# Performance work log

Hardware: AMD Instinct MI355X
Metric: run time of the kernel (lower is better)

## Reference

```python
import jax, jax.numpy as jnp
import numpy as np

TAU = 0.5  # config.tau
EPS = 1e-12  # F.normalize eps


def _pair_idx(n_i, hi):
    # all pairs (i, j) with i in [0, n_i), j in (i, hi)
    ii, jj = [], []
    for i in range(n_i):
        js = np.arange(i + 1, hi)
        ii.append(np.full(js.shape, i))
        jj.append(js)
    return np.concatenate(ii), np.concatenate(jj)


def setup_inputs() -> dict:
    key = jax.random.key(0)
    ks = jax.random.split(key, 7)
    B, D, H = 512, 768, 256
    s = 0.02
    return {
        "emb_in": jax.random.normal(ks[0], (B, D), jnp.float32),
        "W1": jax.random.normal(ks[1], (H, 2 * D), jnp.float32) * s,
        "b1": jax.random.normal(ks[2], (H,), jnp.float32) * s,
        "W2": jax.random.normal(ks[3], (H, H), jnp.float32) * s,
        "b2": jax.random.normal(ks[4], (H,), jnp.float32) * s,
        "W3": jax.random.normal(ks[5], (1, H), jnp.float32) * s,
        "b3": jax.random.normal(ks[6], (1,), jnp.float32) * s,
    }


def reference(emb_in, W1, b1, W2, b2, W3, b3):
    B, D = emb_in.shape
    n = B // 4
    m = B // 2

    # L2 normalize rows (torch F.normalize)
    z = emb_in / jnp.maximum(jnp.linalg.norm(emb_in, axis=1, keepdims=True), EPS)
    # cosine similarity matrix [B, B]
    S = z @ z.T

    # ---- ContrastiveLoss (NT-Xent style over first n rows) ----
    logits = S / jnp.asarray(TAU, emb_in.dtype)
    not_diag = 1.0 - jnp.eye(B, dtype=emb_in.dtype)
    denom = jnp.sum(not_diag * jnp.exp(logits), axis=1)  # sum_{k != i} exp(S[i,k]/T)
    log_denom = jnp.log(denom)  # [B]
    ci, cj = _pair_idx(n, n)  # pairs i < j < n
    # loss_ij = -log( exp(S[i,j]/T) / denom_i ) = log_denom[i] - logits[i, j]
    closs_sum = jnp.sum(log_denom[ci] - logits[ci, cj])
    closs = (-2.0 * (n - 1) / n) * closs_sum

    # ---- en_loss: pairwise concat + tiny MLP + BCEWithLogits ----
    ei_np, ej_np = _pair_idx(n, B)  # pairs i in [0,n), j in (i, B)
    ei = jnp.asarray(ei_np)
    ej = jnp.asarray(ej_np)
    labels = (ej_np < m).astype(np.float32)  # first m-(i+1) pairs per i are positives
    labels = jnp.asarray(labels)

    x = jnp.concatenate([z[ei], z[ej]], axis=1)  # [P, 2D]
    h1 = jax.nn.relu(x @ W1.T + b1)              # [P, H]
    h2 = jax.nn.relu(h1 @ W2.T + b2)             # [P, H]
    logit = (h2 @ W3.T + b3)[:, 0]               # [P]

    # BCEWithLogitsLoss (mean), numerically stable form
    bce = jnp.maximum(logit, 0.0) - logit * labels + jnp.log1p(jnp.exp(-jnp.abs(logit)))
    eloss = jnp.mean(bce)

    return closs + eloss
```

## Files before the change

kernel.cpp:

```cpp
#include <hip/hip_runtime.h>
#include <hip/hip_bf16.h>
#include <math.h>

#define B 512
#define D 768
#define H 256
#define NN 128
#define MM 256
#define P_PAIRS 57280
#define NPBLK 895

typedef __attribute__((ext_vector_type(8))) __bf16 bf16x8;
typedef __attribute__((ext_vector_type(4))) __bf16 bf16x4;
typedef __attribute__((ext_vector_type(4))) float f32x4;


__global__ __launch_bounds__(256) void k_prep(const float* __restrict__ emb,
                                              const float* __restrict__ W1,
                                              const float* __restrict__ W2,
                                              __bf16* __restrict__ zbf,
                                              __bf16* __restrict__ W1b,
                                              __bf16* __restrict__ W2b) {
    int bx = blockIdx.x;
    int t = threadIdx.x;
    if (bx < B) {
        float4 v4 = make_float4(0.f, 0.f, 0.f, 0.f);
        float ss = 0.f;
        if (t < D / 4) {
            v4 = *(const float4*)(emb + bx * D + 4 * t);
            ss = v4.x * v4.x + v4.y * v4.y + v4.z * v4.z + v4.w * v4.w;
        }
        __shared__ float red[256];
        red[t] = ss;
        __syncthreads();
        for (int s = 128; s > 0; s >>= 1) {
            if (t < s) red[t] += red[t + s];
            __syncthreads();
        }
        float inv = 1.0f / fmaxf(sqrtf(red[0]), 1e-12f);
        if (t < D / 4) {
            bf16x4 o;
            o[0] = (__bf16)(v4.x * inv); o[1] = (__bf16)(v4.y * inv);
            o[2] = (__bf16)(v4.z * inv); o[3] = (__bf16)(v4.w * inv);
            *(bf16x4*)(zbf + bx * D + 4 * t) = o;
        }
    } else if (bx < B + 64) {
        int e4 = (bx - B) * 256 + t;
        float4 w = *(const float4*)(W2 + 4 * e4);
        bf16x4 o;
        o[0] = (__bf16)w.x; o[1] = (__bf16)w.y; o[2] = (__bf16)w.z; o[3] = (__bf16)w.w;
        *(bf16x4*)(W2b + 4 * e4) = o;
    } else {
        int n = bx - B - 64;
        if (t < D / 4) {
            float4 w = *(const float4*)(W1 + (n & 255) * (2 * D) + (n >> 8) * D + 4 * t);
            bf16x4 o;
            o[0] = (__bf16)w.x; o[1] = (__bf16)w.y; o[2] = (__bf16)w.z; o[3] = (__bf16)w.w;
            *(bf16x4*)(W1b + n * D + 4 * t) = o;
        }
    }
}

__global__ __launch_bounds__(128) void k_sim_uv(const __bf16* __restrict__ zbf,
                                                const __bf16* __restrict__ W1b,
                                                const float* __restrict__ b1,
                                                __bf16* __restrict__ Up,
                                                __bf16* __restrict__ Vv,
                                                float* __restrict__ esp,
                                                float* __restrict__ slp) {
    int bx = blockIdx.x;
    int w = threadIdx.x >> 6;
    int lane = threadIdx.x & 63;
    int r = lane & 15, q = lane >> 4;

    if (bx < 32) {
        int m0 = (bx >> 2) * 16;
        int n0 = (bx & 3) * 128 + w * 64;
        int slot = (bx & 3) * 2 + w;
        f32x4 acc[4] = {};
        const __bf16* Ab = zbf + (m0 + r) * D + 8 * q;
        #pragma unroll 4
        for (int s = 0; s < D / 32; s++) {
            bf16x8 a = *(const bf16x8*)(Ab + 32 * s);
            #pragma unroll
            for (int nt = 0; nt < 4; nt++) {
                bf16x8 b = *(const bf16x8*)(zbf + (n0 + 16 * nt + r) * D + 8 * q + 32 * s);
                acc[nt] = __builtin_amdgcn_mfma_f32_16x16x32_bf16(a, b, acc[nt], 0, 0, 0);
            }
        }
        #pragma unroll
        for (int rr = 0; rr < 4; rr++) {
            int irow = m0 + q * 4 + rr;
            float es = 0.f, sl = 0.f;
            #pragma unroll
            for (int nt = 0; nt < 4; nt++) {
                int kcol = n0 + nt * 16 + r;
                float C = acc[nt][rr];
                if (kcol != irow) es += expf(2.f * C);
                if (kcol > irow && kcol < NN) sl += 2.f * C;
            }
            #pragma unroll
            for (int m = 1; m <= 8; m <<= 1) {
                es += __shfl_xor(es, m);
                sl += __shfl_xor(sl, m);
            }
            if (r == 0) {
                esp[slot * NN + irow] = es;
                slp[slot * NN + irow] = sl;
            }
        }
    } else {
        int bxu = bx - 32;
        int m0 = (bxu >> 3) * 32 + 16 * w;
        int n0 = (bxu & 7) * 64;
        f32x4 acc[4] = {};
        const __bf16* Ab = zbf + (m0 + r) * D + 8 * q;
        #pragma unroll 4
        for (int s = 0; s < D / 32; s++) {
            bf16x8 a = *(const bf16x8*)(Ab + 32 * s);
            #pragma unroll
            for (int nt = 0; nt < 4; nt++) {
                bf16x8 b = *(const bf16x8*)(W1b + (n0 + 16 * nt + r) * D + 8 * q + 32 * s);
                acc[nt] = __builtin_amdgcn_mfma_f32_16x16x32_bf16(a, b, acc[nt], 0, 0, 0);
            }
        }
        #pragma unroll
        for (int nt = 0; nt < 4; nt++) {
            int n = n0 + 16 * nt + r;
            float bias = (n < H) ? b1[n] : 0.f;
            #pragma unroll
            for (int rr = 0; rr < 4; rr++) {
                int m = m0 + 4 * q + rr;
                float C = acc[nt][rr] + bias;
                if (n < H) Up[m * H + n] = (__bf16)C;
                else       Vv[m * H + (n - H)] = (__bf16)C;
            }
        }
    }
}

__global__ __launch_bounds__(256, 2) void k_pairs(const __bf16* __restrict__ Up,
                                                  const __bf16* __restrict__ Vv,
                                                  const __bf16* __restrict__ W2b,
                                                  const float* __restrict__ b2,
                                                  const float* __restrict__ W3,
                                                  const float* __restrict__ b3,
                                                  float* __restrict__ bcepart) {
    __shared__ __bf16 h1[64][264];
    __shared__ int jj_s[64];
    __shared__ float redbuf[4][64];

    int tid = threadIdx.x;
    int w = tid >> 6, lane = tid & 63;
    int r = lane & 15, q = lane >> 4;
    int p0 = blockIdx.x * 64;

    if (tid < 64) {
        int p = p0 + tid;
        float disc = 1046529.f - 8.f * (float)p;
        int i = (int)((1023.f - sqrtf(disc)) * 0.5f);
        if (i < 0) i = 0;
        if (i > NN - 1) i = NN - 1;
        while (i > 0 && i * (1023 - i) / 2 > p) i--;
        while ((i + 1) * (1022 - i) / 2 <= p) i++;
        int j = i + 1 + (p - i * (1023 - i) / 2);
        jj_s[tid] = (i << 16) | j;
    }
    __syncthreads();

    {
        int t = tid & 63, g = tid >> 6;
        int ij = jj_s[t];
        int i = ij >> 16, j = ij & 0xffff;
        const __bf16* up = Up + i * H + 64 * g;
        const __bf16* vp = Vv + j * H + 64 * g;
        #pragma unroll
        for (int c8 = 0; c8 < 8; c8++) {
            bf16x8 u8 = *(const bf16x8*)(up + 8 * c8);
            bf16x8 v8 = *(const bf16x8*)(vp + 8 * c8);
            bf16x8 hv;
            #pragma unroll
            for (int e = 0; e < 8; e++)
                hv[e] = (__bf16)fmaxf((float)u8[e] + (float)v8[e], 0.f);
            *(bf16x8*)&h1[t][64 * g + 8 * c8] = hv;
        }
    }
    __syncthreads();

    f32x4 acc[4][4] = {};
    const __bf16* wb = W2b + (64 * w + r) * H + 8 * q;
    #pragma unroll
    for (int s = 0; s < 8; s++) {
        bf16x8 a[4], b[4];
        #pragma unroll
        for (int mt = 0; mt < 4; mt++)
            a[mt] = *(const bf16x8*)&h1[16 * mt + r][32 * s + 8 * q];
        #pragma unroll
        for (int nt = 0; nt < 4; nt++)
            b[nt] = *(const bf16x8*)(wb + 16 * nt * H + 32 * s);
        #pragma unroll
        for (int mt = 0; mt < 4; mt++)
            #pragma unroll
            for (int nt = 0; nt < 4; nt++)
                acc[mt][nt] = __builtin_amdgcn_mfma_f32_16x16x32_bf16(a[mt], b[nt], acc[mt][nt], 0, 0, 0);
    }

    float part[4][4] = {};
    #pragma unroll
    for (int nt = 0; nt < 4; nt++) {
        int n = 64 * w + 16 * nt + r;
        float b2v = b2[n], w3v = W3[n];
        #pragma unroll
        for (int mt = 0; mt < 4; mt++)
            #pragma unroll
            for (int rr = 0; rr < 4; rr++) {
                float h2 = fmaxf(acc[mt][nt][rr] + b2v, 0.f);
                part[mt][rr] += h2 * w3v;
            }
    }
    #pragma unroll
    for (int mt = 0; mt < 4; mt++)
        #pragma unroll
        for (int rr = 0; rr < 4; rr++) {
            float v = part[mt][rr];
            #pragma unroll
            for (int m = 1; m <= 8; m <<= 1) v += __shfl_xor(v, m);
            if (r == 0) redbuf[w][16 * mt + 4 * q + rr] = v;
        }
    __syncthreads();

    if (tid < 64) {
        int j = jj_s[tid] & 0xffff;
        float logit = redbuf[0][tid] + redbuf[1][tid] +
                      redbuf[2][tid] + redbuf[3][tid] + b3[0];
        float label = (j < MM) ? 1.f : 0.f;
        float lsum = fmaxf(logit, 0.f) - logit * label +
                     log1pf(expf(-fabsf(logit)));
        #pragma unroll
        for (int off = 32; off > 0; off >>= 1) lsum += __shfl_down(lsum, off);
        if (tid == 0) bcepart[blockIdx.x] = lsum;
    }
}

__global__ __launch_bounds__(256) void k_final(const float* __restrict__ esp,
                                               const float* __restrict__ slp,
                                               const float* __restrict__ bcepart,
                                               float* __restrict__ out) {
    __shared__ float red[256];
    int t = threadIdx.x;

    float s = 0.f;
    for (int p = t; p < NPBLK; p += 256) s += bcepart[p];
    red[t] = s;
    __syncthreads();
    for (int st = 128; st > 0; st >>= 1) {
        if (t < st) red[t] += red[t + st];
        __syncthreads();
    }
    float bce_total = red[0];
    __syncthreads();

    float v = 0.f;
    if (t < NN) {
        float es = 0.f, sl = 0.f;
        #pragma unroll
        for (int s8 = 0; s8 < 8; s8++) {
            es += esp[s8 * NN + t];
            sl += slp[s8 * NN + t];
        }
        v = (float)(NN - 1 - t) * logf(es) - sl;
    }
    red[t] = v;
    __syncthreads();
    for (int st = 128; st > 0; st >>= 1) {
        if (t < st) red[t] += red[t + st];
        __syncthreads();
    }
    if (t == 0) {
        float closs = (-2.0f * (float)(NN - 1) / (float)NN) * red[0];
        out[0] = closs + bce_total / (float)P_PAIRS;
    }
}

extern "C" void kernel_launch(void* const* d_in, const int* in_sizes, int n_in,
                              void* d_out, int out_size, void* d_ws, size_t ws_size,
                              hipStream_t stream) {
    const float* emb = (const float*)d_in[0];
    const float* W1  = (const float*)d_in[1];
    const float* b1  = (const float*)d_in[2];
    const float* W2  = (const float*)d_in[3];
    const float* b2  = (const float*)d_in[4];
    const float* W3  = (const float*)d_in[5];
    const float* b3  = (const float*)d_in[6];
    float* out = (float*)d_out;

    float* ws = (float*)d_ws;
    float* esp     = ws;
    float* slp     = ws + 1024;
    float* bcepart = ws + 2048;
    __bf16* zbf = (__bf16*)(ws + 3072);
    __bf16* W1b = zbf + B * D;
    __bf16* W2b = W1b + 2 * H * D;
    __bf16* Up  = W2b + H * H;
    __bf16* Vv  = Up + B * H;

    k_prep<<<B + 64 + 2 * H, 256, 0, stream>>>(emb, W1, W2, zbf, W1b, W2b);
    k_sim_uv<<<160, 128, 0, stream>>>(zbf, W1b, b1, Up, Vv, esp, slp);
    k_pairs<<<NPBLK, 256, 0, stream>>>(Up, Vv, W2b, b2, W3, b3, bcepart);
    k_final<<<1, 256, 0, stream>>>(esp, slp, bcepart, out);
}
```

Before: 108.6 us.

## Pre-swizzle bf16 operands into MFMA fragment order for coalesced loads

The prep kernel now writes normalized embeddings, W1 and W2 in a fragment-major layout so each MFMA operand load in the similarity/UV and pair kernels is one contiguous 1 KB wavefront read rather than strided row reads. The h1 build in k_pairs is remapped so four adjacent threads cover one pair row, and the occupancy hint is raised from 2 to 4 blocks per CU. The aim is to cut uncoalesced global memory traffic in the GEMM inner loops. The higher occupancy target may force register spills given the 16 accumulator tiles per thread.

```diff
diff --git a/kernel.cpp b/kernel.cpp
--- a/kernel.cpp
+++ b/kernel.cpp
@@ -18,16 +18,17 @@
 __global__ __launch_bounds__(256) void k_prep(const float* __restrict__ emb,
                                               const float* __restrict__ W1,
                                               const float* __restrict__ W2,
-                                              __bf16* __restrict__ zbf,
-                                              __bf16* __restrict__ W1b,
-                                              __bf16* __restrict__ W2b) {
+                                              __bf16* __restrict__ zA,
+                                              __bf16* __restrict__ W1A,
+                                              __bf16* __restrict__ W2s) {
     int bx = blockIdx.x;
     int t = threadIdx.x;
     if (bx < B) {
+        int i = bx;
         float4 v4 = make_float4(0.f, 0.f, 0.f, 0.f);
         float ss = 0.f;
         if (t < D / 4) {
-            v4 = *(const float4*)(emb + bx * D + 4 * t);
+            v4 = *(const float4*)(emb + i * D + 4 * t);
             ss = v4.x * v4.x + v4.y * v4.y + v4.z * v4.z + v4.w * v4.w;
         }
         __shared__ float red[256];
@@ -42,27 +43,34 @@
             bf16x4 o;
             o[0] = (__bf16)(v4.x * inv); o[1] = (__bf16)(v4.y * inv);
             o[2] = (__bf16)(v4.z * inv); o[3] = (__bf16)(v4.w * inv);
-            *(bf16x4*)(zbf + bx * D + 4 * t) = o;
+            int g = i >> 4, r = i & 15;
+            int s24 = t >> 3, q = (t >> 1) & 3, e = (t & 1) * 4;
+            *(bf16x4*)(zA + (((g * 24 + s24) * 64 + q * 16 + r) * 8 + e)) = o;
         }
     } else if (bx < B + 64) {
-        int e4 = (bx - B) * 256 + t;
-        float4 w = *(const float4*)(W2 + 4 * e4);
+        int n = (bx - B) * 4 + (t >> 6);
+        int c = t & 63;
+        float4 w = *(const float4*)(W2 + n * H + 4 * c);
         bf16x4 o;
         o[0] = (__bf16)w.x; o[1] = (__bf16)w.y; o[2] = (__bf16)w.z; o[3] = (__bf16)w.w;
-        *(bf16x4*)(W2b + 4 * e4) = o;
+        int g = n >> 4, r = n & 15;
+        int s8 = c >> 3, q = (c >> 1) & 3, e = (c & 1) * 4;
+        *(bf16x4*)(W2s + (((g * 8 + s8) * 64 + q * 16 + r) * 8 + e)) = o;
     } else {
         int n = bx - B - 64;
         if (t < D / 4) {
             float4 w = *(const float4*)(W1 + (n & 255) * (2 * D) + (n >> 8) * D + 4 * t);
             bf16x4 o;
             o[0] = (__bf16)w.x; o[1] = (__bf16)w.y; o[2] = (__bf16)w.z; o[3] = (__bf16)w.w;
-            *(bf16x4*)(W1b + n * D + 4 * t) = o;
-        }
-    }
-}
-
-__global__ __launch_bounds__(128) void k_sim_uv(const __bf16* __restrict__ zbf,
-                                                const __bf16* __restrict__ W1b,
+            int g = n >> 4, r = n & 15;
+            int s24 = t >> 3, q = (t >> 1) & 3, e = (t & 1) * 4;
+            *(bf16x4*)(W1A + (((g * 24 + s24) * 64 + q * 16 + r) * 8 + e)) = o;
+        }
+    }
+}
+
+__global__ __launch_bounds__(128) void k_sim_uv(const __bf16* __restrict__ zA,
+                                                const __bf16* __restrict__ W1A,
                                                 const float* __restrict__ b1,
                                                 __bf16* __restrict__ Up,
                                                 __bf16* __restrict__ Vv,
@@ -74,27 +82,26 @@
     int r = lane & 15, q = lane >> 4;
 
     if (bx < 32) {
-        int m0 = (bx >> 2) * 16;
-        int n0 = (bx & 3) * 128 + w * 64;
+        int gm = bx >> 2;
+        int gn0 = (bx & 3) * 8 + w * 4;
         int slot = (bx & 3) * 2 + w;
         f32x4 acc[4] = {};
-        const __bf16* Ab = zbf + (m0 + r) * D + 8 * q;
         #pragma unroll 4
         for (int s = 0; s < D / 32; s++) {
-            bf16x8 a = *(const bf16x8*)(Ab + 32 * s);
+            bf16x8 a = *(const bf16x8*)(zA + ((gm * 24 + s) * 64 + lane) * 8);
             #pragma unroll
             for (int nt = 0; nt < 4; nt++) {
-                bf16x8 b = *(const bf16x8*)(zbf + (n0 + 16 * nt + r) * D + 8 * q + 32 * s);
+                bf16x8 b = *(const bf16x8*)(zA + (((gn0 + nt) * 24 + s) * 64 + lane) * 8);
                 acc[nt] = __builtin_amdgcn_mfma_f32_16x16x32_bf16(a, b, acc[nt], 0, 0, 0);
             }
         }
         #pragma unroll
         for (int rr = 0; rr < 4; rr++) {
-            int irow = m0 + q * 4 + rr;
+            int irow = gm * 16 + q * 4 + rr;
             float es = 0.f, sl = 0.f;
             #pragma unroll
             for (int nt = 0; nt < 4; nt++) {
-                int kcol = n0 + nt * 16 + r;
+                int kcol = (gn0 + nt) * 16 + r;
                 float C = acc[nt][rr];
                 if (kcol != irow) es += expf(2.f * C);
                 if (kcol > irow && kcol < NN) sl += 2.f * C;
@@ -111,26 +118,25 @@
         }
     } else {
         int bxu = bx - 32;
-        int m0 = (bxu >> 3) * 32 + 16 * w;
-        int n0 = (bxu & 7) * 64;
+        int gm = (bxu >> 3) * 2 + w;
+        int gn0 = (bxu & 7) * 4;
         f32x4 acc[4] = {};
-        const __bf16* Ab = zbf + (m0 + r) * D + 8 * q;
         #pragma unroll 4
         for (int s = 0; s < D / 32; s++) {
-            bf16x8 a = *(const bf16x8*)(Ab + 32 * s);
+            bf16x8 a = *(const bf16x8*)(zA + ((gm * 24 + s) * 64 + lane) * 8);
             #pragma unroll
             for (int nt = 0; nt < 4; nt++) {
-                bf16x8 b = *(const bf16x8*)(W1b + (n0 + 16 * nt + r) * D + 8 * q + 32 * s);
+                bf16x8 b = *(const bf16x8*)(W1A + (((gn0 + nt) * 24 + s) * 64 + lane) * 8);
                 acc[nt] = __builtin_amdgcn_mfma_f32_16x16x32_bf16(a, b, acc[nt], 0, 0, 0);
             }
         }
         #pragma unroll
         for (int nt = 0; nt < 4; nt++) {
-            int n = n0 + 16 * nt + r;
+            int n = (gn0 + nt) * 16 + r;
             float bias = (n < H) ? b1[n] : 0.f;
             #pragma unroll
             for (int rr = 0; rr < 4; rr++) {
-                int m = m0 + 4 * q + rr;
+                int m = gm * 16 + 4 * q + rr;
                 float C = acc[nt][rr] + bias;
                 if (n < H) Up[m * H + n] = (__bf16)C;
                 else       Vv[m * H + (n - H)] = (__bf16)C;
@@ -139,9 +145,9 @@
     }
 }
 
-__global__ __launch_bounds__(256, 2) void k_pairs(const __bf16* __restrict__ Up,
+__global__ __launch_bounds__(256, 4) void k_pairs(const __bf16* __restrict__ Up,
                                                   const __bf16* __restrict__ Vv,
-                                                  const __bf16* __restrict__ W2b,
+                                                  const __bf16* __restrict__ W2s,
                                                   const float* __restrict__ b2,
                                                   const float* __restrict__ W3,
                                                   const float* __restrict__ b3,
@@ -169,11 +175,12 @@
     __syncthreads();
 
     {
-        int t = tid & 63, g = tid >> 6;
-        int ij = jj_s[t];
+        int row = tid >> 2;
+        int cq = tid & 3;
+        int ij = jj_s[row];
         int i = ij >> 16, j = ij & 0xffff;
-        const __bf16* up = Up + i * H + 64 * g;
-        const __bf16* vp = Vv + j * H + 64 * g;
+        const __bf16* up = Up + i * H + 64 * cq;
+        const __bf16* vp = Vv + j * H + 64 * cq;
         #pragma unroll
         for (int c8 = 0; c8 < 8; c8++) {
             bf16x8 u8 = *(const bf16x8*)(up + 8 * c8);
@@ -182,13 +189,12 @@
             #pragma unroll
             for (int e = 0; e < 8; e++)
                 hv[e] = (__bf16)fmaxf((float)u8[e] + (float)v8[e], 0.f);
-            *(bf16x8*)&h1[t][64 * g + 8 * c8] = hv;
+            *(bf16x8*)&h1[row][64 * cq + 8 * c8] = hv;
         }
     }
     __syncthreads();
 
     f32x4 acc[4][4] = {};
-    const __bf16* wb = W2b + (64 * w + r) * H + 8 * q;
     #pragma unroll
     for (int s = 0; s < 8; s++) {
         bf16x8 a[4], b[4];
@@ -197,7 +203,7 @@
             a[mt] = *(const bf16x8*)&h1[16 * mt + r][32 * s + 8 * q];
         #pragma unroll
         for (int nt = 0; nt < 4; nt++)
-            b[nt] = *(const bf16x8*)(wb + 16 * nt * H + 32 * s);
+            b[nt] = *(const bf16x8*)(W2s + (((4 * w + nt) * 8 + s) * 64 + lane) * 8);
         #pragma unroll
         for (int mt = 0; mt < 4; mt++)
             #pragma unroll
@@ -298,14 +304,14 @@
     float* esp     = ws;
     float* slp     = ws + 1024;
     float* bcepart = ws + 2048;
-    __bf16* zbf = (__bf16*)(ws + 3072);
-    __bf16* W1b = zbf + B * D;
-    __bf16* W2b = W1b + 2 * H * D;
-    __bf16* Up  = W2b + H * H;
+    __bf16* zA  = (__bf16*)(ws + 3072);
+    __bf16* W1A = zA + B * D;
+    __bf16* W2s = W1A + 2 * H * D;
+    __bf16* Up  = W2s + H * H;
     __bf16* Vv  = Up + B * H;
 
-    k_prep<<<B + 64 + 2 * H, 256, 0, stream>>>(emb, W1, W2, zbf, W1b, W2b);
-    k_sim_uv<<<160, 128, 0, stream>>>(zbf, W1b, b1, Up, Vv, esp, slp);
-    k_pairs<<<NPBLK, 256, 0, stream>>>(Up, Vv, W2b, b2, W3, b3, bcepart);
+    k_prep<<<B + 64 + 2 * H, 256, 0, stream>>>(emb, W1, W2, zA, W1A, W2s);
+    k_sim_uv<<<160, 128, 0, stream>>>(zA, W1A, b1, Up, Vv, esp, slp);
+    k_pairs<<<NPBLK, 256, 0, stream>>>(Up, Vv, W2s, b2, W3, b3, bcepart);
     k_final<<<1, 256, 0, stream>>>(esp, slp, bcepart, out);
 }
```

Measured after the change: 103.2 us. 5.0% less time.
